# Optimization experiments

Hardware: AMD Instinct MI355X
Metric: run time of the kernel (lower is better)

## Reference

```python
import jax, jax.numpy as jnp
import numpy as np

B, T, D = 256, 512, 256

def setup_inputs() -> dict:
    key = jax.random.key(0)
    k1, k2, k3, k4 = jax.random.split(key, 4)
    ip = jax.random.normal(k1, (B, T, D), dtype=jnp.float32)
    W = jax.random.normal(k2, (D, D), dtype=jnp.float32) * (1.0 / np.sqrt(D))
    b = jax.random.normal(k3, (D,), dtype=jnp.float32) * 0.05
    context = jax.random.normal(k4, (D, 1), dtype=jnp.float32) * 0.05
    return {"ip": ip, "W": W, "b": b, "context": context}

def reference(ip, W, b, context) -> jnp.ndarray:
    # linear -> tanh: [B, T, D]
    h = jnp.tanh(jnp.einsum("btd,ed->bte", ip, W) + b)
    # attention scores over words: [B, T]
    scores = jnp.einsum("btd,d->bt", h, context[:, 0])
    attn = jax.nn.softmax(scores, axis=1)
    # weighted sum over words -> sentence embeddings: [B, D]
    sent_embeds = jnp.einsum("bt,btd->bd", attn, ip)
    return sent_embeds
```

## Files before the change

kernel.cpp:

```cpp
#include <hip/hip_runtime.h>
#include <hip/hip_bf16.h>

#define NBATCH 256
#define NT 512
#define ND 256
#define NROWS (NBATCH * NT)

typedef __attribute__((ext_vector_type(8))) short short8;
typedef __attribute__((ext_vector_type(4))) float floatx4;

__device__ __forceinline__ unsigned short f2bf(float x) {
    unsigned int u = __float_as_uint(x);
    u += 0x7FFFu + ((u >> 16) & 1u);
    return (unsigned short)(u >> 16);
}

__global__ void __launch_bounds__(256) prep_kernel(
    const float* __restrict__ W, unsigned short* __restrict__ wbf)
{
    int i = (blockIdx.x * 256 + threadIdx.x) * 4;
    float4 f = *(const float4*)(W + i);
    ushort4 o;
    o.x = f2bf(f.x); o.y = f2bf(f.y); o.z = f2bf(f.z); o.w = f2bf(f.w);
    *(ushort4*)(wbf + i) = o;
}

__global__ void __launch_bounds__(256, 2) scores_kernel(
    const float* __restrict__ ip,
    const unsigned short* __restrict__ wbf,
    const float* __restrict__ bias,
    const float* __restrict__ ctx,
    float* __restrict__ scores)
{
    __shared__ __align__(16) char wsm[32768];
    __shared__ float bias_s[ND];
    __shared__ float ctx_s[ND];

    const int tid  = threadIdx.x;
    const int lane = tid & 63;
    const int wv   = tid >> 6;
    const int m    = lane & 15;
    const int q    = lane >> 4;
    const long row0 = (long)blockIdx.x * 128 + wv * 32;

    bias_s[tid] = bias[tid];
    ctx_s[tid]  = ctx[tid];

    short8 a[2][8];
#pragma unroll
    for (int tile = 0; tile < 2; ++tile) {
        const float* ar = ip + (row0 + tile * 16 + m) * ND + q * 8;
#pragma unroll
        for (int s = 0; s < 8; ++s) {
            float4 f0 = *(const float4*)(ar + s * 32);
            float4 f1 = *(const float4*)(ar + s * 32 + 4);
            short8 v;
            v[0] = (short)f2bf(f0.x); v[1] = (short)f2bf(f0.y);
            v[2] = (short)f2bf(f0.z); v[3] = (short)f2bf(f0.w);
            v[4] = (short)f2bf(f1.x); v[5] = (short)f2bf(f1.y);
            v[6] = (short)f2bf(f1.z); v[7] = (short)f2bf(f1.w);
            a[tile][s] = v;
        }
    }

    float sc0[4] = {0.f, 0.f, 0.f, 0.f};
    float sc1[4] = {0.f, 0.f, 0.f, 0.f};
    const short8* wch = (const short8*)wbf;

#pragma unroll 1
    for (int stage = 0; stage < 4; ++stage) {
        if (stage) __syncthreads();
#pragma unroll
        for (int u = 0; u < 8; ++u) {
            int c  = stage * 2048 + tid + u * 256;
            int cm = c & 15, cq = (c >> 4) & 3, cs = (c >> 6) & 7, cnb = c >> 9;
            int G  = ((cnb * 16 + cm) << 5) + cq + (cs << 2);
            *(short8*)(wsm + ((tid + u * 256) << 4)) = wch[G];
        }
        __syncthreads();

#pragma unroll 1
        for (int nbl = 0; nbl < 4; ++nbl) {
            const int e  = (stage * 4 + nbl) * 16 + m;
            const char* wbase = wsm + (((nbl << 9) + lane) << 4);
            short8 w[8];
#pragma unroll
            for (int s = 0; s < 8; ++s)
                w[s] = *(const short8*)(wbase + (s << 10));
            floatx4 acc0 = {0.f, 0.f, 0.f, 0.f};
            floatx4 acc1 = {0.f, 0.f, 0.f, 0.f};
#pragma unroll
            for (int s = 0; s < 8; ++s) {
                acc0 = __builtin_amdgcn_mfma_f32_16x16x32_bf16(a[0][s], w[s], acc0, 0, 0, 0);
                acc1 = __builtin_amdgcn_mfma_f32_16x16x32_bf16(a[1][s], w[s], acc1, 0, 0, 0);
            }
            const float be = bias_s[e];
            const float ce = ctx_s[e];
#pragma unroll
            for (int r = 0; r < 4; ++r) {
                float x0 = acc0[r] + be;
                float x1 = acc1[r] + be;
                sc0[r] += (1.f - 2.f / (__expf(2.f * x0) + 1.f)) * ce;
                sc1[r] += (1.f - 2.f / (__expf(2.f * x1) + 1.f)) * ce;
            }
        }
    }

#pragma unroll
    for (int off = 8; off >= 1; off >>= 1) {
#pragma unroll
        for (int r = 0; r < 4; ++r) {
            sc0[r] += __shfl_xor(sc0[r], off, 64);
            sc1[r] += __shfl_xor(sc1[r], off, 64);
        }
    }
    if (m == 0) {
#pragma unroll
        for (int r = 0; r < 4; ++r) {
            scores[row0 + q * 4 + r]      = sc0[r];
            scores[row0 + 16 + q * 4 + r] = sc1[r];
        }
    }
}

__global__ void __launch_bounds__(256) wsum_kernel(
    const float* __restrict__ ip,
    const float* __restrict__ scores,
    float* __restrict__ out)
{
    __shared__ float attn_s[NT];
    __shared__ float red[8];
    __shared__ float partial[16][64];

    const int b  = blockIdx.x >> 2;
    const int dq = blockIdx.x & 3;
    const int tid  = threadIdx.x;
    const int lane = tid & 63;
    const int wv   = tid >> 6;

    float s0 = scores[(long)b * NT + tid];
    float s1 = scores[(long)b * NT + tid + 256];
    float mx = fmaxf(s0, s1);
#pragma unroll
    for (int off = 32; off >= 1; off >>= 1) mx = fmaxf(mx, __shfl_xor(mx, off, 64));
    if (lane == 0) red[wv] = mx;
    __syncthreads();
    mx = fmaxf(fmaxf(red[0], red[1]), fmaxf(red[2], red[3]));
    float e0 = __expf(s0 - mx), e1 = __expf(s1 - mx);
    float sm = e0 + e1;
#pragma unroll
    for (int off = 32; off >= 1; off >>= 1) sm += __shfl_xor(sm, off, 64);
    __syncthreads();
    if (lane == 0) red[4 + wv] = sm;
    __syncthreads();
    sm = red[4] + red[5] + red[6] + red[7];
    float inv = 1.f / sm;
    attn_s[tid]       = e0 * inv;
    attn_s[tid + 256] = e1 * inv;
    __syncthreads();

    const int dg = tid & 15;
    const int ts = tid >> 4;
    const float4* base = (const float4*)(ip + (long)b * NT * ND + dq * 64) + dg;
    float a0 = 0.f, a1 = 0.f, a2 = 0.f, a3 = 0.f;
#pragma unroll 8
    for (int t = ts * 32; t < ts * 32 + 32; ++t) {
        float w = attn_s[t];
        float4 v = base[t * 64];
        a0 += w * v.x; a1 += w * v.y; a2 += w * v.z; a3 += w * v.w;
    }
    partial[ts][dg * 4 + 0] = a0;
    partial[ts][dg * 4 + 1] = a1;
    partial[ts][dg * 4 + 2] = a2;
    partial[ts][dg * 4 + 3] = a3;
    __syncthreads();
    if (tid < 64) {
        float r = 0.f;
#pragma unroll
        for (int i = 0; i < 16; ++i) r += partial[i][tid];
        out[(long)b * ND + dq * 64 + tid] = r;
    }
}

extern "C" void kernel_launch(void* const* d_in, const int* in_sizes, int n_in,
                              void* d_out, int out_size, void* d_ws, size_t ws_size,
                              hipStream_t stream) {
    const float* ip   = (const float*)d_in[0];
    const float* W    = (const float*)d_in[1];
    const float* bias = (const float*)d_in[2];
    const float* ctx  = (const float*)d_in[3];

    unsigned short* wbf = (unsigned short*)d_ws;
    float* scores = (float*)((char*)d_ws + ND * ND * sizeof(unsigned short));

    prep_kernel<<<64, 256, 0, stream>>>(W, wbf);
    scores_kernel<<<NROWS / 128, 256, 0, stream>>>(ip, wbf, bias, ctx, scores);
    wsum_kernel<<<NBATCH * 4, 256, 0, stream>>>(ip, scores, (float*)d_out);
}
```

Before: 241.1 us.

## Pre-swizzle W into MFMA fragment layout and read it directly from global

The prep kernel now writes W in bf16 already permuted into the per-lane MFMA B-fragment order. The scores kernel drops its shared-memory staging and the block barriers, loading the weight fragments straight from global (L2/L1-resident) memory, and reads bias and context directly. The tanh-times-context is rewritten with a hardware reciprocal and a fused multiply-add, and the occupancy hint rises from two to three blocks per CU. The risk is more global/L1 traffic per wave and extra register pressure under the tighter launch bound.

```diff
diff --git a/kernel.cpp b/kernel.cpp
--- a/kernel.cpp
+++ b/kernel.cpp
@@ -16,35 +16,34 @@
 }
 
 __global__ void __launch_bounds__(256) prep_kernel(
-    const float* __restrict__ W, unsigned short* __restrict__ wbf)
+    const float* __restrict__ W, unsigned short* __restrict__ wf)
 {
-    int i = (blockIdx.x * 256 + threadIdx.x) * 4;
-    float4 f = *(const float4*)(W + i);
-    ushort4 o;
-    o.x = f2bf(f.x); o.y = f2bf(f.y); o.z = f2bf(f.z); o.w = f2bf(f.w);
-    *(ushort4*)(wbf + i) = o;
+    int g  = blockIdx.x * 256 + threadIdx.x;
+    int m  = g & 15, q = (g >> 4) & 3, s = (g >> 6) & 7, nb = g >> 9;
+    const float* src = W + (nb * 16 + m) * ND + q * 8 + s * 32;
+    float4 f0 = *(const float4*)src;
+    float4 f1 = *(const float4*)(src + 4);
+    short8 v;
+    v[0] = (short)f2bf(f0.x); v[1] = (short)f2bf(f0.y);
+    v[2] = (short)f2bf(f0.z); v[3] = (short)f2bf(f0.w);
+    v[4] = (short)f2bf(f1.x); v[5] = (short)f2bf(f1.y);
+    v[6] = (short)f2bf(f1.z); v[7] = (short)f2bf(f1.w);
+    *(short8*)(wf + (long)g * 8) = v;
 }
 
-__global__ void __launch_bounds__(256, 2) scores_kernel(
+__global__ void __launch_bounds__(256, 3) scores_kernel(
     const float* __restrict__ ip,
-    const unsigned short* __restrict__ wbf,
+    const unsigned short* __restrict__ wf,
     const float* __restrict__ bias,
     const float* __restrict__ ctx,
     float* __restrict__ scores)
 {
-    __shared__ __align__(16) char wsm[32768];
-    __shared__ float bias_s[ND];
-    __shared__ float ctx_s[ND];
-
     const int tid  = threadIdx.x;
     const int lane = tid & 63;
     const int wv   = tid >> 6;
     const int m    = lane & 15;
     const int q    = lane >> 4;
     const long row0 = (long)blockIdx.x * 128 + wv * 32;
-
-    bias_s[tid] = bias[tid];
-    ctx_s[tid]  = ctx[tid];
 
     short8 a[2][8];
 #pragma unroll
@@ -65,44 +64,33 @@
 
     float sc0[4] = {0.f, 0.f, 0.f, 0.f};
     float sc1[4] = {0.f, 0.f, 0.f, 0.f};
-    const short8* wch = (const short8*)wbf;
+    const short8* wchunks = (const short8*)wf;
 
 #pragma unroll 1
-    for (int stage = 0; stage < 4; ++stage) {
-        if (stage) __syncthreads();
+    for (int nb = 0; nb < 16; ++nb) {
+        const int e = nb * 16 + m;
+        const short8* wp = wchunks + nb * 512 + lane;
+        short8 w[8];
 #pragma unroll
-        for (int u = 0; u < 8; ++u) {
-            int c  = stage * 2048 + tid + u * 256;
-            int cm = c & 15, cq = (c >> 4) & 3, cs = (c >> 6) & 7, cnb = c >> 9;
-            int G  = ((cnb * 16 + cm) << 5) + cq + (cs << 2);
-            *(short8*)(wsm + ((tid + u * 256) << 4)) = wch[G];
+        for (int s = 0; s < 8; ++s) w[s] = wp[s * 64];
+        floatx4 acc0 = {0.f, 0.f, 0.f, 0.f};
+        floatx4 acc1 = {0.f, 0.f, 0.f, 0.f};
+#pragma unroll
+        for (int s = 0; s < 8; ++s) {
+            acc0 = __builtin_amdgcn_mfma_f32_16x16x32_bf16(a[0][s], w[s], acc0, 0, 0, 0);
+            acc1 = __builtin_amdgcn_mfma_f32_16x16x32_bf16(a[1][s], w[s], acc1, 0, 0, 0);
         }
-        __syncthreads();
-
-#pragma unroll 1
-        for (int nbl = 0; nbl < 4; ++nbl) {
-            const int e  = (stage * 4 + nbl) * 16 + m;
-            const char* wbase = wsm + (((nbl << 9) + lane) << 4);
-            short8 w[8];
+        const float be  = bias[e];
+        const float ce  = ctx[e];
+        const float ce2 = ce + ce;
 #pragma unroll
-            for (int s = 0; s < 8; ++s)
-                w[s] = *(const short8*)(wbase + (s << 10));
-            floatx4 acc0 = {0.f, 0.f, 0.f, 0.f};
-            floatx4 acc1 = {0.f, 0.f, 0.f, 0.f};
-#pragma unroll
-            for (int s = 0; s < 8; ++s) {
-                acc0 = __builtin_amdgcn_mfma_f32_16x16x32_bf16(a[0][s], w[s], acc0, 0, 0, 0);
-                acc1 = __builtin_amdgcn_mfma_f32_16x16x32_bf16(a[1][s], w[s], acc1, 0, 0, 0);
-            }
-            const float be = bias_s[e];
-            const float ce = ctx_s[e];
-#pragma unroll
-            for (int r = 0; r < 4; ++r) {
-                float x0 = acc0[r] + be;
-                float x1 = acc1[r] + be;
-                sc0[r] += (1.f - 2.f / (__expf(2.f * x0) + 1.f)) * ce;
-                sc1[r] += (1.f - 2.f / (__expf(2.f * x1) + 1.f)) * ce;
-            }
+        for (int r = 0; r < 4; ++r) {
+            float x0 = acc0[r] + be;
+            float x1 = acc1[r] + be;
+            float t0 = __builtin_amdgcn_rcpf(__expf(x0 + x0) + 1.f);
+            float t1 = __builtin_amdgcn_rcpf(__expf(x1 + x1) + 1.f);
+            sc0[r] = __builtin_fmaf(-ce2, t0, sc0[r] + ce);
+            sc1[r] = __builtin_fmaf(-ce2, t1, sc1[r] + ce);
         }
     }
 
@@ -190,10 +178,10 @@
     const float* bias = (const float*)d_in[2];
     const float* ctx  = (const float*)d_in[3];
 
-    unsigned short* wbf = (unsigned short*)d_ws;
+    unsigned short* wf = (unsigned short*)d_ws;
     float* scores = (float*)((char*)d_ws + ND * ND * sizeof(unsigned short));
 
-    prep_kernel<<<64, 256, 0, stream>>>(W, wbf);
-    scores_kernel<<<NROWS / 128, 256, 0, stream>>>(ip, wbf, bias, ctx, scores);
+    prep_kernel<<<32, 256, 0, stream>>>(W, wf);
+    scores_kernel<<<NROWS / 128, 256, 0, stream>>>(ip, wf, bias, ctx, scores);
     wsum_kernel<<<NBATCH * 4, 256, 0, stream>>>(ip, scores, (float*)d_out);
 }
```

Measured after the change: 241.4 us. Within noise of the previous version (+0.1%).
